# Kernel optimization log

Hardware: AMD Instinct MI355X
Metric: run time of the kernel (lower is better)

The kernel has to match this reference:

```python
import jax, jax.numpy as jnp
import numpy as np

H = 2048      # hidden size
E = 16        # num experts
F = 1408      # per-expert ffn
FS = 4096     # shared expert ffn
B, S = 2, 1024


def setup_inputs() -> dict:
    key = jax.random.key(0)
    ks = jax.random.split(key, 9)
    s = 0.02
    x = jax.random.normal(ks[0], (B, S, H), dtype=jnp.float32)
    w_router = jax.random.normal(ks[1], (E, H), dtype=jnp.float32) * s
    Wg = jax.random.normal(ks[2], (E, H, F), dtype=jnp.float32) * s
    Wu = jax.random.normal(ks[3], (E, H, F), dtype=jnp.float32) * s
    Wd = jax.random.normal(ks[4], (E, F, H), dtype=jnp.float32) * s
    Wg_s = jax.random.normal(ks[5], (H, FS), dtype=jnp.float32) * s
    Wu_s = jax.random.normal(ks[6], (H, FS), dtype=jnp.float32) * s
    Wd_s = jax.random.normal(ks[7], (FS, H), dtype=jnp.float32) * s
    return {"x": x, "w_router": w_router, "Wg": Wg, "Wu": Wu, "Wd": Wd,
            "Wg_s": Wg_s, "Wu_s": Wu_s, "Wd_s": Wd_s, "top_k": 4}


def reference(x, w_router, Wg, Wu, Wd, Wg_s, Wu_s, Wd_s, top_k):
    # router: softmax in fp32, top-k, renormalize
    logits = jnp.einsum('bsh,eh->bse', x, w_router)
    probs = jax.nn.softmax(logits.astype(jnp.float32), axis=-1)
    w, idx = jax.lax.top_k(probs, top_k)            # [B,S,K]
    w = w / jnp.sum(w, axis=-1, keepdims=True)
    # per-token weight per expert; top-k experts are distinct, so the
    # per-slot masked loop in torch collapses to a single mask [B,S,E]
    mask = jnp.sum(jax.nn.one_hot(idx, E, dtype=w.dtype) * w[..., None], axis=-2)
    out = jnp.zeros_like(x)
    for e in range(E):
        m = mask[..., e:e + 1]                      # [B,S,1]
        xi = x * m                                  # input scaled by routing weight (matches torch)
        h = jax.nn.silu(jnp.einsum('bsh,hf->bsf', xi, Wg[e])) \
            * jnp.einsum('bsh,hf->bsf', xi, Wu[e])
        out = out + jnp.einsum('bsf,fh->bsh', h, Wd[e]) * m
    # shared expert (always active, unscaled)
    hs = jax.nn.silu(jnp.einsum('bsh,hf->bsf', x, Wg_s)) \
         * jnp.einsum('bsh,hf->bsf', x, Wu_s)
    out = out + jnp.einsum('bsf,fh->bsh', hs, Wd_s)
    return out
```

## Files before the change

### kernel.cpp

```cpp
#include <hip/hip_runtime.h>

#define H 2048
#define E 16
#define F 1408
#define FS 4096
#define T 2048
#define TOPK 4
#define CAP 2048
#define NPADROWS (T * TOPK + E * 128)
#define NMB (NPADROWS / 128)
#define NS ((FS / 128) * (T / 128))
#define GS1 (NS + (F / 128) * NMB)
#define GS2E ((H / 128) * NMB)

typedef __bf16 bf16;
typedef bf16 bf16x4 __attribute__((ext_vector_type(4)));
typedef bf16 bf16x8 __attribute__((ext_vector_type(8)));
typedef float floatx4 __attribute__((ext_vector_type(4)));

static __device__ __forceinline__ floatx4 mfma16(bf16x8 a, bf16x8 b, floatx4 c) {
    return __builtin_amdgcn_mfma_f32_16x16x32_bf16(a, b, c, 0, 0, 0);
}

static __device__ __forceinline__ void gload16(const bf16* g, bf16* l) {
    __builtin_amdgcn_global_load_lds(
        (const __attribute__((address_space(1))) void*)g,
        (__attribute__((address_space(3))) void*)l, 16, 0, 0);
}

__global__ __launch_bounds__(256) void router_kernel(
    const float* __restrict__ x, const float* __restrict__ wr,
    int* __restrict__ cnt, int* __restrict__ tokid, float* __restrict__ tokw) {
    const int wave = threadIdx.x >> 6;
    const int lane = threadIdx.x & 63;
    const int t = blockIdx.x * 4 + wave;
    if (t >= T) return;
    const float* xrow = x + (size_t)t * H;
    float xr[H / 64];
#pragma unroll
    for (int i = 0; i < H / 64; i++) xr[i] = xrow[lane + i * 64];
    float logits[E];
    for (int e = 0; e < E; e++) {
        const float* wrow = wr + (size_t)e * H;
        float p = 0.f;
#pragma unroll
        for (int i = 0; i < H / 64; i++) p += xr[i] * wrow[lane + i * 64];
        for (int off = 32; off; off >>= 1) p += __shfl_xor(p, off, 64);
        logits[e] = p;
    }
    float mx = logits[0];
    for (int e = 1; e < E; e++) mx = fmaxf(mx, logits[e]);
    float pr[E];
    float sum = 0.f;
    for (int e = 0; e < E; e++) { pr[e] = __expf(logits[e] - mx); sum += pr[e]; }
    float inv = 1.f / sum;
    for (int e = 0; e < E; e++) pr[e] *= inv;
    int sel[TOPK]; float sw[TOPK]; float wsum = 0.f;
    for (int k = 0; k < TOPK; k++) {
        float best = -1.f; int bi = 0;
        for (int e = 0; e < E; e++) if (pr[e] > best) { best = pr[e]; bi = e; }
        sel[k] = bi; sw[k] = best; wsum += best; pr[bi] = -2.f;
    }
    if (lane == 0) {
        float invw = 1.f / wsum;
        for (int k = 0; k < TOPK; k++) {
            int e = sel[k];
            int pos = atomicAdd(&cnt[e], 1);
            tokid[e * CAP + pos] = t;
            tokw[e * CAP + pos] = sw[k] * invw;
        }
    }
}

__global__ void prefix_kernel(const int* __restrict__ cnt, int* __restrict__ prefix) {
    if (threadIdx.x == 0) {
        int s = 0;
        for (int e = 0; e < E; e++) { prefix[e] = s; s += (cnt[e] + 127) & ~127; }
        prefix[E] = s;
    }
}

__global__ __launch_bounds__(256) void convert_x(const float* __restrict__ x,
                                                 bf16* __restrict__ Xb) {
    const int t = threadIdx.x;
    const int row = blockIdx.x * 8 + (t >> 5);
    const int l32 = t & 31;
    const float* src = x + (size_t)row * H;
    bf16* dst = Xb + (size_t)row * H;
    const int xk = (row & 7) << 3;
#pragma unroll
    for (int i = 0; i < 8; i++) {
        int kb = l32 * 8 + i * 256;
        float4 a = *(const float4*)(src + kb);
        float4 b = *(const float4*)(src + kb + 4);
        bf16x8 v;
        v[0] = (bf16)a.x; v[1] = (bf16)a.y; v[2] = (bf16)a.z; v[3] = (bf16)a.w;
        v[4] = (bf16)b.x; v[5] = (bf16)b.y; v[6] = (bf16)b.z; v[7] = (bf16)b.w;
        *(bf16x8*)(dst + (kb ^ xk)) = v;
    }
}

__global__ __launch_bounds__(256) void gather_x(
    const float* __restrict__ x, const int* __restrict__ cnt,
    const int* __restrict__ prefixPad, const int* __restrict__ tokid,
    const float* __restrict__ tokw, bf16* __restrict__ Xg) {
    const int e = blockIdx.y;
    const int s0 = blockIdx.x * 8;
    const int n = cnt[e];
    if (s0 >= n) return;
    const int t = threadIdx.x;
    const int sl = s0 + (t >> 5);
    const int l32 = t & 31;
    if (sl >= n) return;
    const int tok = tokid[e * CAP + sl];
    const float w = tokw[e * CAP + sl];
    const int row = prefixPad[e] + sl;
    const float* src = x + (size_t)tok * H;
    bf16* dst = Xg + (size_t)row * H;
    const int xk = (row & 7) << 3;
#pragma unroll
    for (int i = 0; i < 8; i++) {
        int kb = l32 * 8 + i * 256;
        float4 a = *(const float4*)(src + kb);
        float4 b = *(const float4*)(src + kb + 4);
        bf16x8 v;
        v[0] = (bf16)(a.x * w); v[1] = (bf16)(a.y * w);
        v[2] = (bf16)(a.z * w); v[3] = (bf16)(a.w * w);
        v[4] = (bf16)(b.x * w); v[5] = (bf16)(b.y * w);
        v[6] = (bf16)(b.z * w); v[7] = (bf16)(b.w * w);
        *(bf16x8*)(dst + (kb ^ xk)) = v;
    }
}

__global__ __launch_bounds__(256) void transpose_cvt(
    const float* __restrict__ src, bf16* __restrict__ dst, int R, int C) {
    __shared__ float tile[64][33];
    const int t = threadIdx.x;
    const size_t zb = (size_t)blockIdx.z * R * C;
    const int r0 = blockIdx.y * 64, c0 = blockIdx.x * 32;
    {
        const int rl = t >> 2, c8 = (t & 3) * 8;
        const float* s = src + zb + (size_t)(r0 + rl) * C + c0 + c8;
        float4 v0 = *(const float4*)s;
        float4 v1 = *(const float4*)(s + 4);
        tile[rl][c8 + 0] = v0.x; tile[rl][c8 + 1] = v0.y;
        tile[rl][c8 + 2] = v0.z; tile[rl][c8 + 3] = v0.w;
        tile[rl][c8 + 4] = v1.x; tile[rl][c8 + 5] = v1.y;
        tile[rl][c8 + 6] = v1.z; tile[rl][c8 + 7] = v1.w;
    }
    __syncthreads();
    {
        const int cl = t >> 3, r8 = (t & 7) * 8;
        bf16x8 o;
#pragma unroll
        for (int i = 0; i < 8; i++) o[i] = (bf16)tile[r8 + i][cl];
        const int cg = c0 + cl;
        *(bf16x8*)(dst + zb + (size_t)cg * R + ((r0 + r8) ^ ((cg & 7) << 3))) = o;
    }
}

__global__ __launch_bounds__(256, 2) void s1_all(
    const bf16* __restrict__ Xb, const bf16* __restrict__ Xg,
    const bf16* __restrict__ WgsT, const bf16* __restrict__ WusT,
    const bf16* __restrict__ WgT, const bf16* __restrict__ WuT,
    bf16* __restrict__ Hs, bf16* __restrict__ Hb,
    const int* __restrict__ cnt, const int* __restrict__ prefixPad) {
    __shared__ __align__(16) bf16 As[128 * 64];
    __shared__ __align__(16) bf16 Bgs[128 * 64];
    __shared__ __align__(16) bf16 Bus[128 * 64];

    const int raw = blockIdx.x;
    const int id = (raw & 7) * (GS1 / 8) + (raw >> 3);

    int n0, m0, ne, nF;
    const bf16 *A, *bg, *bu;
    bf16* hb;
    if (id < NS) {
        m0 = (id & 15) * 128;
        n0 = (id >> 4) * 128;
        ne = 1 << 30;
        nF = FS;
        A = Xb; bg = WgsT; bu = WusT; hb = Hs;
    } else {
        const int id2 = id - NS;
        const int mb = id2 % NMB;
        const int xx = id2 / NMB;
        const int rowbase = mb * 128;
        if (rowbase >= prefixPad[E]) return;
        int e = 0;
        while (prefixPad[e + 1] <= rowbase) e++;
        const int pp = prefixPad[e];
        m0 = rowbase - pp;
        ne = cnt[e];
        n0 = xx * 128;
        nF = F;
        A = Xg + (size_t)pp * H;
        bg = WgT + (size_t)e * F * H;
        bu = WuT + (size_t)e * F * H;
        hb = Hb + (size_t)pp * F;
    }

    const int tid = threadIdx.x;
    const int lane = tid & 63;
    const int wave = tid >> 6;
    const bf16* aP = A + (size_t)(m0 + wave * 32 + (lane >> 3)) * H + (lane & 7) * 8;
    const bf16* gP = bg + (size_t)(n0 + wave * 32 + (lane >> 3)) * H + (lane & 7) * 8;
    const bf16* uP = bu + (size_t)(n0 + wave * 32 + (lane >> 3)) * H + (lane & 7) * 8;

    const int m_ = lane & 15;
    const int quad = lane >> 4;
    const int wm = (wave & 1) * 64;
    const int wn = (wave >> 1) * 64;

    floatx4 accg[4][4], accu[4][4];
#pragma unroll
    for (int i = 0; i < 4; i++)
#pragma unroll
        for (int j = 0; j < 4; j++) {
            accg[i][j] = (floatx4){0.f, 0.f, 0.f, 0.f};
            accu[i][j] = (floatx4){0.f, 0.f, 0.f, 0.f};
        }

    for (int k0 = 0; k0 < H; k0 += 64) {
#pragma unroll
        for (int j = 0; j < 4; j++) {
            gload16(aP + k0 + (size_t)j * 8 * H, &As[wave * 2048 + j * 512]);
            gload16(gP + k0 + (size_t)j * 8 * H, &Bgs[wave * 2048 + j * 512]);
            gload16(uP + k0 + (size_t)j * 8 * H, &Bus[wave * 2048 + j * 512]);
        }
        __syncthreads();
#pragma unroll
        for (int kk = 0; kk < 2; kk++) {
            const int ko = (((kk << 2) | quad) ^ (m_ & 7)) << 3;
            bf16x8 af[4], bgf[4], buf_[4];
#pragma unroll
            for (int mi = 0; mi < 4; mi++)
                af[mi] = *(const bf16x8*)&As[(wm + mi * 16 + m_) * 64 + ko];
#pragma unroll
            for (int ni = 0; ni < 4; ni++) {
                bgf[ni] = *(const bf16x8*)&Bgs[(wn + ni * 16 + m_) * 64 + ko];
                buf_[ni] = *(const bf16x8*)&Bus[(wn + ni * 16 + m_) * 64 + ko];
            }
#pragma unroll
            for (int mi = 0; mi < 4; mi++)
#pragma unroll
                for (int ni = 0; ni < 4; ni++) {
                    accg[mi][ni] = mfma16(af[mi], bgf[ni], accg[mi][ni]);
                    accu[mi][ni] = mfma16(af[mi], buf_[ni], accu[mi][ni]);
                }
        }
        __syncthreads();
    }

#pragma unroll
    for (int mi = 0; mi < 4; mi++)
#pragma unroll
        for (int ni = 0; ni < 4; ni++)
#pragma unroll
            for (int r = 0; r < 4; r++) {
                int row = m0 + wm + mi * 16 + quad * 4 + r;
                int col = n0 + wn + ni * 16 + m_;
                if (row < ne) {
                    float g = accg[mi][ni][r];
                    float u = accu[mi][ni][r];
                    float hv = g / (1.f + __expf(-g)) * u;
                    hb[(size_t)row * nF + (col ^ ((row & 7) << 3))] = (bf16)hv;
                }
            }
}

template <bool EXPERT>
__global__ __launch_bounds__(256, 2) void s2_gemm(
    const bf16* __restrict__ hin, const bf16* __restrict__ BdT,
    float* __restrict__ out, const int* __restrict__ cnt,
    const int* __restrict__ prefixPad, const int* __restrict__ tokid,
    const float* __restrict__ tokw, int nK) {
    __shared__ __align__(16) bf16 As[128 * 64];
    __shared__ __align__(16) bf16 Bs[128 * 64];
    const int raw = blockIdx.x;
    const int id = EXPERT ? (raw & 7) * (GS2E / 8) + (raw >> 3)
                          : (raw & 7) * 32 + (raw >> 3);
    int n0, m0, ne, e = 0;
    const bf16 *A, *B;
    if (EXPERT) {
        const int mb = id % NMB;
        const int xx = id / NMB;
        const int rowbase = mb * 128;
        if (rowbase >= prefixPad[E]) return;
        while (prefixPad[e + 1] <= rowbase) e++;
        const int pp = prefixPad[e];
        m0 = rowbase - pp;
        ne = cnt[e];
        n0 = xx * 128;
        A = hin + (size_t)pp * F;
        B = BdT + (size_t)e * F * H;
    } else {
        m0 = (id & 15) * 128;
        n0 = (id >> 4) * 128;
        ne = 1 << 30;
        A = hin; B = BdT;
    }
    const int tid = threadIdx.x;
    const int lane = tid & 63;
    const int wave = tid >> 6;
    const bf16* aP = A + (size_t)(m0 + wave * 32 + (lane >> 3)) * nK + (lane & 7) * 8;
    const bf16* bP = B + (size_t)(n0 + wave * 32 + (lane >> 3)) * nK + (lane & 7) * 8;

    const int m_ = lane & 15;
    const int quad = lane >> 4;
    const int wm = (wave & 1) * 64;
    const int wn = (wave >> 1) * 64;

    floatx4 acc[4][4];
#pragma unroll
    for (int i = 0; i < 4; i++)
#pragma unroll
        for (int j = 0; j < 4; j++) acc[i][j] = (floatx4){0.f, 0.f, 0.f, 0.f};

    for (int k0 = 0; k0 < nK; k0 += 64) {
#pragma unroll
        for (int j = 0; j < 4; j++) {
            gload16(aP + k0 + (size_t)j * 8 * nK, &As[wave * 2048 + j * 512]);
            gload16(bP + k0 + (size_t)j * 8 * nK, &Bs[wave * 2048 + j * 512]);
        }
        __syncthreads();
#pragma unroll
        for (int kk = 0; kk < 2; kk++) {
            const int ko = (((kk << 2) | quad) ^ (m_ & 7)) << 3;
            bf16x8 af[4], bf_[4];
#pragma unroll
            for (int mi = 0; mi < 4; mi++)
                af[mi] = *(const bf16x8*)&As[(wm + mi * 16 + m_) * 64 + ko];
#pragma unroll
            for (int ni = 0; ni < 4; ni++)
                bf_[ni] = *(const bf16x8*)&Bs[(wn + ni * 16 + m_) * 64 + ko];
#pragma unroll
            for (int mi = 0; mi < 4; mi++)
#pragma unroll
                for (int ni = 0; ni < 4; ni++)
                    acc[mi][ni] = mfma16(af[mi], bf_[ni], acc[mi][ni]);
        }
        __syncthreads();
    }

#pragma unroll
    for (int mi = 0; mi < 4; mi++)
#pragma unroll
        for (int ni = 0; ni < 4; ni++)
#pragma unroll
            for (int r = 0; r < 4; r++) {
                int row = m0 + wm + mi * 16 + quad * 4 + r;
                int col = n0 + wn + ni * 16 + m_;
                if (EXPERT) {
                    if (row < ne) {
                        int t = tokid[e * CAP + row];
                        float wgt = tokw[e * CAP + row];
                        atomicAdd(out + (size_t)t * H + col, acc[mi][ni][r] * wgt);
                    }
                } else {
                    out[(size_t)row * H + col] = acc[mi][ni][r];
                }
            }
}

extern "C" void kernel_launch(void* const* d_in, const int* in_sizes, int n_in,
                              void* d_out, int out_size, void* d_ws, size_t ws_size,
                              hipStream_t stream) {
    const float* x = (const float*)d_in[0];
    const float* w_router = (const float*)d_in[1];
    const float* Wg = (const float*)d_in[2];
    const float* Wu = (const float*)d_in[3];
    const float* Wd = (const float*)d_in[4];
    const float* Wg_s = (const float*)d_in[5];
    const float* Wu_s = (const float*)d_in[6];
    const float* Wd_s = (const float*)d_in[7];
    float* out = (float*)d_out;

    char* w = (char*)d_ws;
    int* cnt = (int*)(w + 0);
    int* prefix = (int*)(w + 64);
    int* tokid = (int*)(w + 256);
    float* tokw = (float*)(w + 256 + (size_t)E * CAP * 4);

    constexpr size_t OFF_XB = 262400;
    constexpr size_t OFF_XG = OFF_XB + (size_t)T * H * 2;
    constexpr size_t OFF_HS = OFF_XG + (size_t)NPADROWS * H * 2;
    constexpr size_t OFF_HB = OFF_HS + (size_t)T * FS * 2;
    constexpr size_t OFF_WGT = OFF_HB + (size_t)NPADROWS * F * 2;
    constexpr size_t OFF_WUT = OFF_WGT + (size_t)E * F * H * 2;
    constexpr size_t OFF_WDT = OFF_WUT + (size_t)E * F * H * 2;
    constexpr size_t OFF_WGS = OFF_WDT + (size_t)E * F * H * 2;
    constexpr size_t OFF_WUS = OFF_WGS + (size_t)H * FS * 2;
    constexpr size_t OFF_WDS = OFF_WUS + (size_t)H * FS * 2;

    bf16* Xb = (bf16*)(w + OFF_XB);
    bf16* Xg = (bf16*)(w + OFF_XG);
    bf16* Hs = (bf16*)(w + OFF_HS);
    bf16* Hb = (bf16*)(w + OFF_HB);
    bf16* WgT = (bf16*)(w + OFF_WGT);
    bf16* WuT = (bf16*)(w + OFF_WUT);
    bf16* WdT = (bf16*)(w + OFF_WDT);
    bf16* WgsT = (bf16*)(w + OFF_WGS);
    bf16* WusT = (bf16*)(w + OFF_WUS);
    bf16* WdsT = (bf16*)(w + OFF_WDS);

    hipMemsetAsync(cnt, 0, 64, stream);
    router_kernel<<<T / 4, 256, 0, stream>>>(x, w_router, cnt, tokid, tokw);
    prefix_kernel<<<1, 64, 0, stream>>>(cnt, prefix);

    convert_x<<<T / 8, 256, 0, stream>>>(x, Xb);
    gather_x<<<dim3(CAP / 8, E), 256, 0, stream>>>(x, cnt, prefix, tokid, tokw, Xg);
    transpose_cvt<<<dim3(F / 32, H / 64, E), 256, 0, stream>>>(Wg, WgT, H, F);
    transpose_cvt<<<dim3(F / 32, H / 64, E), 256, 0, stream>>>(Wu, WuT, H, F);
    transpose_cvt<<<dim3(H / 32, F / 64, E), 256, 0, stream>>>(Wd, WdT, F, H);
    transpose_cvt<<<dim3(FS / 32, H / 64, 1), 256, 0, stream>>>(Wg_s, WgsT, H, FS);
    transpose_cvt<<<dim3(FS / 32, H / 64, 1), 256, 0, stream>>>(Wu_s, WusT, H, FS);
    transpose_cvt<<<dim3(H / 32, FS / 64, 1), 256, 0, stream>>>(Wd_s, WdsT, FS, H);

    s1_all<<<GS1, 256, 0, stream>>>(Xb, Xg, WgsT, WusT, WgT, WuT, Hs, Hb, cnt, prefix);

    s2_gemm<false><<<(H / 128) * (T / 128), 256, 0, stream>>>(
        Hs, WdsT, out, nullptr, nullptr, nullptr, nullptr, FS);
    s2_gemm<true><<<GS2E, 256, 0, stream>>>(
        Hb, WdT, out, cnt, prefix, tokid, tokw, F);
}
```

Measured before the change: 1.175 ms.

## Fuse weight prep, merge down-proj GEMMs, replace atomics with partial-sum reduction

The six transpose/convert launches and the x conversion are merged into one prep kernel that uses 64x64 tiles. The shared and expert down-projection GEMMs become a single launch. The expert path no longer does float atomicAdd into the output. It writes weighted rows into a partial buffer that reuses the WgT workspace, and a new final_add kernel sums each token's top-k rows into out using a per-token slot map recorded by the router. Occupancy hints on s1/s2 are also raised. The aim is to cut launch overhead and atomic contention, at the cost of an extra pass over an fp32 partial buffer of roughly 84 MB.

```diff
diff --git a/kernel.cpp b/kernel.cpp
--- a/kernel.cpp
+++ b/kernel.cpp
@@ -11,7 +11,14 @@
 #define NMB (NPADROWS / 128)
 #define NS ((FS / 128) * (T / 128))
 #define GS1 (NS + (F / 128) * NMB)
-#define GS2E ((H / 128) * NMB)
+#define GS2 ((H / 128) * (T / 128) + (H / 128) * NMB)
+
+#define TPE ((H / 64) * (F / 64))
+#define NT_E (E * TPE)
+#define TS_GU ((H / 64) * (FS / 64))
+#define TS_D ((FS / 64) * (H / 64))
+#define PREP_TR (3 * NT_E + 2 * TS_GU + TS_D)
+#define PREP_GRID (PREP_TR + T / 8)
 
 typedef __bf16 bf16;
 typedef bf16 bf16x4 __attribute__((ext_vector_type(4)));
@@ -30,7 +37,8 @@
 
 __global__ __launch_bounds__(256) void router_kernel(
     const float* __restrict__ x, const float* __restrict__ wr,
-    int* __restrict__ cnt, int* __restrict__ tokid, float* __restrict__ tokw) {
+    int* __restrict__ cnt, int* __restrict__ tokid, float* __restrict__ tokw,
+    int* __restrict__ tokslot) {
     const int wave = threadIdx.x >> 6;
     const int lane = threadIdx.x & 63;
     const int t = blockIdx.x * 4 + wave;
@@ -68,6 +76,7 @@
             int pos = atomicAdd(&cnt[e], 1);
             tokid[e * CAP + pos] = t;
             tokw[e * CAP + pos] = sw[k] * invw;
+            tokslot[t * TOPK + k] = (e << 16) | pos;
         }
     }
 }
@@ -80,23 +89,87 @@
     }
 }
 
-__global__ __launch_bounds__(256) void convert_x(const float* __restrict__ x,
-                                                 bf16* __restrict__ Xb) {
+__global__ __launch_bounds__(256) void prep_kernel(
+    const float* __restrict__ Wg, const float* __restrict__ Wu,
+    const float* __restrict__ Wd, const float* __restrict__ Wgs,
+    const float* __restrict__ Wus, const float* __restrict__ Wds,
+    const float* __restrict__ x,
+    bf16* __restrict__ WgT, bf16* __restrict__ WuT, bf16* __restrict__ WdT,
+    bf16* __restrict__ WgsT, bf16* __restrict__ WusT, bf16* __restrict__ WdsT,
+    bf16* __restrict__ Xb) {
+    __shared__ float tile[64][65];
+    const int id = blockIdx.x;
     const int t = threadIdx.x;
-    const int row = blockIdx.x * 8 + (t >> 5);
-    const int l32 = t & 31;
-    const float* src = x + (size_t)row * H;
-    bf16* dst = Xb + (size_t)row * H;
-    const int xk = (row & 7) << 3;
-#pragma unroll
-    for (int i = 0; i < 8; i++) {
-        int kb = l32 * 8 + i * 256;
-        float4 a = *(const float4*)(src + kb);
-        float4 b = *(const float4*)(src + kb + 4);
-        bf16x8 v;
-        v[0] = (bf16)a.x; v[1] = (bf16)a.y; v[2] = (bf16)a.z; v[3] = (bf16)a.w;
-        v[4] = (bf16)b.x; v[5] = (bf16)b.y; v[6] = (bf16)b.z; v[7] = (bf16)b.w;
-        *(bf16x8*)(dst + (kb ^ xk)) = v;
+    if (id >= PREP_TR) {
+        const int row = (id - PREP_TR) * 8 + (t >> 5);
+        const int l32 = t & 31;
+        const float* src = x + (size_t)row * H;
+        bf16* dst = Xb + (size_t)row * H;
+        const int xk = (row & 7) << 3;
+#pragma unroll
+        for (int i = 0; i < 8; i++) {
+            int kb = l32 * 8 + i * 256;
+            float4 a = *(const float4*)(src + kb);
+            float4 b = *(const float4*)(src + kb + 4);
+            bf16x8 v;
+            v[0] = (bf16)a.x; v[1] = (bf16)a.y; v[2] = (bf16)a.z; v[3] = (bf16)a.w;
+            v[4] = (bf16)b.x; v[5] = (bf16)b.y; v[6] = (bf16)b.z; v[7] = (bf16)b.w;
+            *(bf16x8*)(dst + (kb ^ xk)) = v;
+        }
+        return;
+    }
+    const float* src; bf16* dst; int R, C, r0, c0;
+    size_t zoff = 0;
+    if (id < 2 * NT_E) {
+        const int which = id / NT_E;
+        const int rem = id % NT_E;
+        const int e = rem / TPE, tl = rem % TPE;
+        R = H; C = F;
+        r0 = (tl / (F / 64)) * 64; c0 = (tl % (F / 64)) * 64;
+        src = which ? Wu : Wg; dst = which ? WuT : WgT;
+        zoff = (size_t)e * H * F;
+    } else if (id < 3 * NT_E) {
+        const int rem = id - 2 * NT_E;
+        const int e = rem / TPE, tl = rem % TPE;
+        R = F; C = H;
+        r0 = (tl / (H / 64)) * 64; c0 = (tl % (H / 64)) * 64;
+        src = Wd; dst = WdT;
+        zoff = (size_t)e * F * H;
+    } else if (id < 3 * NT_E + 2 * TS_GU) {
+        const int rem = id - 3 * NT_E;
+        const int which = rem / TS_GU, tl = rem % TS_GU;
+        R = H; C = FS;
+        r0 = (tl / (FS / 64)) * 64; c0 = (tl % (FS / 64)) * 64;
+        src = which ? Wus : Wgs; dst = which ? WusT : WgsT;
+    } else {
+        const int tl = id - 3 * NT_E - 2 * TS_GU;
+        R = FS; C = H;
+        r0 = (tl / (H / 64)) * 64; c0 = (tl % (H / 64)) * 64;
+        src = Wds; dst = WdsT;
+    }
+    {
+        const int rl = t >> 2, cq = (t & 3) * 16;
+        const float* s = src + zoff + (size_t)(r0 + rl) * C + c0 + cq;
+        float4 v0 = ((const float4*)s)[0];
+        float4 v1 = ((const float4*)s)[1];
+        float4 v2 = ((const float4*)s)[2];
+        float4 v3 = ((const float4*)s)[3];
+        float* tr = &tile[rl][cq];
+        tr[0] = v0.x; tr[1] = v0.y; tr[2] = v0.z; tr[3] = v0.w;
+        tr[4] = v1.x; tr[5] = v1.y; tr[6] = v1.z; tr[7] = v1.w;
+        tr[8] = v2.x; tr[9] = v2.y; tr[10] = v2.z; tr[11] = v2.w;
+        tr[12] = v3.x; tr[13] = v3.y; tr[14] = v3.z; tr[15] = v3.w;
+    }
+    __syncthreads();
+#pragma unroll
+    for (int p = 0; p < 2; p++) {
+        const int cl = p * 32 + (t >> 3);
+        const int r8 = (t & 7) * 8;
+        bf16x8 o;
+#pragma unroll
+        for (int i = 0; i < 8; i++) o[i] = (bf16)tile[r8 + i][cl];
+        const int cg = c0 + cl;
+        *(bf16x8*)(dst + zoff + (size_t)cg * R + ((r0 + r8) ^ ((cg & 7) << 3))) = o;
     }
 }
 
@@ -132,34 +205,7 @@
     }
 }
 
-__global__ __launch_bounds__(256) void transpose_cvt(
-    const float* __restrict__ src, bf16* __restrict__ dst, int R, int C) {
-    __shared__ float tile[64][33];
-    const int t = threadIdx.x;
-    const size_t zb = (size_t)blockIdx.z * R * C;
-    const int r0 = blockIdx.y * 64, c0 = blockIdx.x * 32;
-    {
-        const int rl = t >> 2, c8 = (t & 3) * 8;
-        const float* s = src + zb + (size_t)(r0 + rl) * C + c0 + c8;
-        float4 v0 = *(const float4*)s;
-        float4 v1 = *(const float4*)(s + 4);
-        tile[rl][c8 + 0] = v0.x; tile[rl][c8 + 1] = v0.y;
-        tile[rl][c8 + 2] = v0.z; tile[rl][c8 + 3] = v0.w;
-        tile[rl][c8 + 4] = v1.x; tile[rl][c8 + 5] = v1.y;
-        tile[rl][c8 + 6] = v1.z; tile[rl][c8 + 7] = v1.w;
-    }
-    __syncthreads();
-    {
-        const int cl = t >> 3, r8 = (t & 7) * 8;
-        bf16x8 o;
-#pragma unroll
-        for (int i = 0; i < 8; i++) o[i] = (bf16)tile[r8 + i][cl];
-        const int cg = c0 + cl;
-        *(bf16x8*)(dst + zb + (size_t)cg * R + ((r0 + r8) ^ ((cg & 7) << 3))) = o;
-    }
-}
-
-__global__ __launch_bounds__(256, 2) void s1_all(
+__global__ __launch_bounds__(256, 3) void s1_all(
     const bf16* __restrict__ Xb, const bf16* __restrict__ Xg,
     const bf16* __restrict__ WgsT, const bf16* __restrict__ WusT,
     const bf16* __restrict__ WgT, const bf16* __restrict__ WuT,
@@ -269,36 +315,38 @@
             }
 }
 
-template <bool EXPERT>
-__global__ __launch_bounds__(256, 2) void s2_gemm(
-    const bf16* __restrict__ hin, const bf16* __restrict__ BdT,
-    float* __restrict__ out, const int* __restrict__ cnt,
-    const int* __restrict__ prefixPad, const int* __restrict__ tokid,
-    const float* __restrict__ tokw, int nK) {
+__global__ __launch_bounds__(256, 4) void s2_all(
+    const bf16* __restrict__ Hs, const bf16* __restrict__ Hb,
+    const bf16* __restrict__ WdsT, const bf16* __restrict__ WdT,
+    float* __restrict__ out, float* __restrict__ partial,
+    const int* __restrict__ cnt, const int* __restrict__ prefixPad,
+    const float* __restrict__ tokw) {
     __shared__ __align__(16) bf16 As[128 * 64];
     __shared__ __align__(16) bf16 Bs[128 * 64];
     const int raw = blockIdx.x;
-    const int id = EXPERT ? (raw & 7) * (GS2E / 8) + (raw >> 3)
-                          : (raw & 7) * 32 + (raw >> 3);
-    int n0, m0, ne, e = 0;
+    const int id = (raw & 7) * (GS2 / 8) + (raw >> 3);
+    int n0, m0, ne, nK, e = 0, pp = 0;
     const bf16 *A, *B;
-    if (EXPERT) {
-        const int mb = id % NMB;
-        const int xx = id / NMB;
+    bool expert;
+    if (id < (H / 128) * (T / 128)) {
+        m0 = (id & 15) * 128;
+        n0 = (id >> 4) * 128;
+        ne = 1 << 30;
+        A = Hs; B = WdsT; nK = FS; expert = false;
+    } else {
+        const int id2 = id - (H / 128) * (T / 128);
+        const int mb = id2 % NMB;
+        const int xx = id2 / NMB;
         const int rowbase = mb * 128;
         if (rowbase >= prefixPad[E]) return;
         while (prefixPad[e + 1] <= rowbase) e++;
-        const int pp = prefixPad[e];
+        pp = prefixPad[e];
         m0 = rowbase - pp;
         ne = cnt[e];
         n0 = xx * 128;
-        A = hin + (size_t)pp * F;
-        B = BdT + (size_t)e * F * H;
-    } else {
-        m0 = (id & 15) * 128;
-        n0 = (id >> 4) * 128;
-        ne = 1 << 30;
-        A = hin; B = BdT;
+        A = Hb + (size_t)pp * F;
+        B = WdT + (size_t)e * F * H;
+        nK = F; expert = true;
     }
     const int tid = threadIdx.x;
     const int lane = tid & 63;
@@ -351,16 +399,40 @@
             for (int r = 0; r < 4; r++) {
                 int row = m0 + wm + mi * 16 + quad * 4 + r;
                 int col = n0 + wn + ni * 16 + m_;
-                if (EXPERT) {
+                if (expert) {
                     if (row < ne) {
-                        int t = tokid[e * CAP + row];
                         float wgt = tokw[e * CAP + row];
-                        atomicAdd(out + (size_t)t * H + col, acc[mi][ni][r] * wgt);
+                        partial[(size_t)(pp + row) * H + col] = acc[mi][ni][r] * wgt;
                     }
                 } else {
                     out[(size_t)row * H + col] = acc[mi][ni][r];
                 }
             }
+}
+
+__global__ __launch_bounds__(256) void final_add(
+    float* __restrict__ out, const float* __restrict__ partial,
+    const int* __restrict__ tokslot, const int* __restrict__ prefixPad) {
+    const int t = blockIdx.x;
+    const int tid = threadIdx.x;
+    int prow[TOPK];
+#pragma unroll
+    for (int k = 0; k < TOPK; k++) {
+        int s = tokslot[t * TOPK + k];
+        prow[k] = prefixPad[s >> 16] + (s & 0xffff);
+    }
+    float4* o = (float4*)(out + (size_t)t * H);
+#pragma unroll
+    for (int i = 0; i < H / 4 / 256; i++) {
+        int idx = tid + i * 256;
+        float4 v = o[idx];
+#pragma unroll
+        for (int k = 0; k < TOPK; k++) {
+            float4 p = ((const float4*)(partial + (size_t)prow[k] * H))[idx];
+            v.x += p.x; v.y += p.y; v.z += p.z; v.w += p.w;
+        }
+        o[idx] = v;
+    }
 }
 
 extern "C" void kernel_launch(void* const* d_in, const int* in_sizes, int n_in,
@@ -382,7 +454,8 @@
     int* tokid = (int*)(w + 256);
     float* tokw = (float*)(w + 256 + (size_t)E * CAP * 4);
 
-    constexpr size_t OFF_XB = 262400;
+    constexpr size_t OFF_TOKSLOT = 262400;
+    constexpr size_t OFF_XB = OFF_TOKSLOT + (size_t)T * TOPK * 4;
     constexpr size_t OFF_XG = OFF_XB + (size_t)T * H * 2;
     constexpr size_t OFF_HS = OFF_XG + (size_t)NPADROWS * H * 2;
     constexpr size_t OFF_HB = OFF_HS + (size_t)T * FS * 2;
@@ -393,6 +466,7 @@
     constexpr size_t OFF_WUS = OFF_WGS + (size_t)H * FS * 2;
     constexpr size_t OFF_WDS = OFF_WUS + (size_t)H * FS * 2;
 
+    int* tokslot = (int*)(w + OFF_TOKSLOT);
     bf16* Xb = (bf16*)(w + OFF_XB);
     bf16* Xg = (bf16*)(w + OFF_XG);
     bf16* Hs = (bf16*)(w + OFF_HS);
@@ -403,24 +477,16 @@
     bf16* WgsT = (bf16*)(w + OFF_WGS);
     bf16* WusT = (bf16*)(w + OFF_WUS);
     bf16* WdsT = (bf16*)(w + OFF_WDS);
+    float* partial = (float*)(w + OFF_WGT);
 
     hipMemsetAsync(cnt, 0, 64, stream);
-    router_kernel<<<T / 4, 256, 0, stream>>>(x, w_router, cnt, tokid, tokw);
+    router_kernel<<<T / 4, 256, 0, stream>>>(x, w_router, cnt, tokid, tokw, tokslot);
     prefix_kernel<<<1, 64, 0, stream>>>(cnt, prefix);
-
-    convert_x<<<T / 8, 256, 0, stream>>>(x, Xb);
     gather_x<<<dim3(CAP / 8, E), 256, 0, stream>>>(x, cnt, prefix, tokid, tokw, Xg);
-    transpose_cvt<<<dim3(F / 32, H / 64, E), 256, 0, stream>>>(Wg, WgT, H, F);
-    transpose_cvt<<<dim3(F / 32, H / 64, E), 256, 0, stream>>>(Wu, WuT, H, F);
-    transpose_cvt<<<dim3(H / 32, F / 64, E), 256, 0, stream>>>(Wd, WdT, F, H);
-    transpose_cvt<<<dim3(FS / 32, H / 64, 1), 256, 0, stream>>>(Wg_s, WgsT, H, FS);
-    transpose_cvt<<<dim3(FS / 32, H / 64, 1), 256, 0, stream>>>(Wu_s, WusT, H, FS);
-    transpose_cvt<<<dim3(H / 32, FS / 64, 1), 256, 0, stream>>>(Wd_s, WdsT, FS, H);
+    prep_kernel<<<PREP_GRID, 256, 0, stream>>>(Wg, Wu, Wd, Wg_s, Wu_s, Wd_s, x,
+                                               WgT, WuT, WdT, WgsT, WusT, WdsT, Xb);
 
     s1_all<<<GS1, 256, 0, stream>>>(Xb, Xg, WgsT, WusT, WgT, WuT, Hs, Hb, cnt, prefix);
-
-    s2_gemm<false><<<(H / 128) * (T / 128), 256, 0, stream>>>(
-        Hs, WdsT, out, nullptr, nullptr, nullptr, nullptr, FS);
-    s2_gemm<true><<<GS2E, 256, 0, stream>>>(
-        Hb, WdT, out, cnt, prefix, tokid, tokw, F);
-}
+    s2_all<<<GS2, 256, 0, stream>>>(Hs, Hb, WdsT, WdT, out, partial, cnt, prefix, tokw);
+    final_add<<<T, 256, 0, stream>>>(out, partial, tokslot, prefix);
+}
```

New measurement: 1.535 ms. +30.7%, slower.
